# Optimization experiments

Measured on AMD Instinct MI355X. Metric: run time of the kernel, lower is better.

## Reference

```python
import jax, jax.numpy as jnp
import numpy as np

D_MODEL = 1024
D_STATE = 64
HEADDIM = 64
EXPAND = 2
D_INNER = D_MODEL * EXPAND          # 2048
NHEADS = D_INNER // HEADDIM          # 32
D_IN_PROJ = 2 * D_INNER + 2 * D_STATE + NHEADS  # 4256
BATCH, SEQLEN = 4, 4096


def layernorm(x, w, b, eps=1e-5):
    mu = jnp.mean(x, axis=-1, keepdims=True)
    var = jnp.mean(jnp.square(x - mu), axis=-1, keepdims=True)
    return (x - mu) * jax.lax.rsqrt(var + eps) * w + b


def setup_inputs() -> dict:
    key = jax.random.key(0)
    ks = jax.random.split(key, 5)
    x = jax.random.normal(ks[0], (BATCH, SEQLEN, D_MODEL), dtype=jnp.float32)
    # xavier-ish small init (gain 0.5) as in _init_weights
    in_proj_w = jax.random.normal(ks[1], (D_IN_PROJ, D_MODEL), dtype=jnp.float32) * 0.5 * np.sqrt(2.0 / (D_IN_PROJ + D_MODEL))
    out_proj_w = jax.random.normal(ks[2], (D_MODEL, D_INNER), dtype=jnp.float32) * 0.5 * np.sqrt(2.0 / (D_MODEL + D_INNER))
    A_log = jnp.log(jnp.arange(1, NHEADS + 1, dtype=jnp.float32))
    dt_bias = jax.random.normal(ks[3], (NHEADS,), dtype=jnp.float32) * 0.01 + 0.1
    Dparam = jnp.ones((NHEADS,), dtype=jnp.float32)
    return {
        'x': x, 'in_proj_w': in_proj_w, 'out_proj_w': out_proj_w,
        'A_log': A_log, 'dt_bias': dt_bias, 'Dparam': Dparam,
        'ln_w': jnp.ones((D_INNER,), jnp.float32), 'ln_b': jnp.zeros((D_INNER,), jnp.float32),
        'ni_w': jnp.ones((D_MODEL,), jnp.float32), 'ni_b': jnp.zeros((D_MODEL,), jnp.float32),
        'no_w': jnp.ones((D_MODEL,), jnp.float32), 'no_b': jnp.zeros((D_MODEL,), jnp.float32),
    }


def _selective_scan(x_multi, A, Bm, Cm, dt):
    # x_multi: [B,L,H,P], A: [H], Bm/Cm: [B,L,N], dt: [B,L,H]
    Bb, L, H, P = x_multi.shape
    N = Bm.shape[-1]
    dA = jnp.minimum(jnp.exp(dt * A[None, None, :]), 0.99)  # [B,L,H]

    def step(h, inp):
        x_t, B_t, C_t, dA_t = inp  # [B,H,P], [B,N], [B,N], [B,H]
        dBx = jnp.einsum('bhp,bn->bhpn', x_t, B_t)
        h = jnp.clip(dA_t[:, :, None, None] * h + dBx, -10.0, 10.0)
        y_t = jnp.einsum('bn,bhpn->bhp', C_t, h)
        return h, y_t

    h0 = jnp.zeros((Bb, H, P, N), dtype=x_multi.dtype)
    xs = (jnp.moveaxis(x_multi, 1, 0), jnp.moveaxis(Bm, 1, 0),
          jnp.moveaxis(Cm, 1, 0), jnp.moveaxis(dA, 1, 0))
    _, y = jax.lax.scan(step, h0, xs)  # y: [L,B,H,P]
    return jnp.moveaxis(y, 0, 1)


def reference(x, in_proj_w, out_proj_w, A_log, dt_bias, Dparam,
              ln_w, ln_b, ni_w, ni_b, no_w, no_b):
    Bb, L, Dm = x.shape
    x_norm = layernorm(x, ni_w, ni_b)
    zxbcdt = jnp.einsum('bld,ed->ble', x_norm, in_proj_w)  # [B,L,D_IN_PROJ]
    z = zxbcdt[..., :D_INNER]
    x_ssm = zxbcdt[..., D_INNER:2 * D_INNER]
    Bm = zxbcdt[..., 2 * D_INNER:2 * D_INNER + D_STATE]
    Cm = zxbcdt[..., 2 * D_INNER + D_STATE:2 * D_INNER + 2 * D_STATE]
    dt = zxbcdt[..., 2 * D_INNER + 2 * D_STATE:]
    dt = jnp.clip(jax.nn.softplus(dt + dt_bias[None, None, :]), 0.001, 0.1)  # [B,L,H]
    A = -jnp.exp(A_log)  # [H]
    x_multi = x_ssm.reshape(Bb, L, NHEADS, HEADDIM)
    y = _selective_scan(x_multi, A, Bm, Cm, dt)  # [B,L,H,P]
    y = y + x_multi * Dparam[None, None, :, None]  # D skip
    y = y.reshape(Bb, L, D_INNER)
    y = y * jax.nn.silu(z)
    y = layernorm(y, ln_w, ln_b)
    y = jnp.einsum('ble,de->bld', y, out_proj_w)
    y = jnp.clip(y, -10.0, 10.0)
    y = layernorm(y, no_w, no_b)
    return y
```

## Files before the change

kernel.cpp:

```cpp
#include <hip/hip_runtime.h>
#include <hip/hip_bf16.h>
#include <stdint.h>

typedef _Float16 F16;
typedef F16 f16x8 __attribute__((ext_vector_type(8)));
typedef F16 f16x4 __attribute__((ext_vector_type(4)));
typedef float f32x4 __attribute__((ext_vector_type(4)));

#define NTOK   16384
#define DMODEL 1024
#define DINNER 2048
#define DSTATE 64
#define NHEADS 32
#define DINPRJ 4256
#define SEQLEN_ 4096
#define SEGLEN 128
#define NSEG   32

__device__ __forceinline__ void load_lds16(const void* g, void* l) {
  __builtin_amdgcn_global_load_lds((__attribute__((address_space(1))) void*)g,
                                   (__attribute__((address_space(3))) void*)l,
                                   16, 0, 0);
}

__device__ __forceinline__ void lds_st8(F16* base, int row, int col, int rowbytes, f16x8 v) {
  int by = (row * rowbytes + col * 2) ^ ((row & 7) << 4);
  *(f16x8*)((char*)base + by) = v;
}
__device__ __forceinline__ void lds_st1(F16* base, int row, int col, int rowbytes, F16 v) {
  int by = (row * rowbytes + col * 2) ^ ((row & 7) << 4);
  *(F16*)((char*)base + by) = v;
}
__device__ __forceinline__ f16x8 lds_ld8(const F16* base, int row, int col, int rowbytes) {
  int by = (row * rowbytes + col * 2) ^ ((row & 7) << 4);
  return *(const f16x8*)((const char*)base + by);
}

__global__ __launch_bounds__(256) void cvt_kernel(const float* __restrict__ src,
                                                  F16* __restrict__ dst, int n4) {
  int i = blockIdx.x * 256 + threadIdx.x;
  if (i >= n4) return;
  float4 v = *(const float4*)(src + (size_t)i * 4);
  f16x4 o = { (F16)v.x, (F16)v.y, (F16)v.z, (F16)v.w };
  *(f16x4*)(dst + (size_t)i * 4) = o;
}

__device__ __forceinline__ void blk_reduce2(float& s, float& ss) {
  __shared__ float red[8];
#pragma unroll
  for (int m = 32; m >= 1; m >>= 1) { s += __shfl_xor(s, m, 64); ss += __shfl_xor(ss, m, 64); }
  int tid = threadIdx.x, wv = tid >> 6;
  if ((tid & 63) == 0) { red[wv * 2] = s; red[wv * 2 + 1] = ss; }
  __syncthreads();
  s  = red[0] + red[2] + red[4] + red[6];
  ss = red[1] + red[3] + red[5] + red[7];
}

__global__ __launch_bounds__(256) void ln_in_kernel(const float* __restrict__ x,
                                                    const float* __restrict__ w,
                                                    const float* __restrict__ b,
                                                    F16* __restrict__ out) {
  int row = blockIdx.x, tid = threadIdx.x;
  const float* xr = x + (size_t)row * DMODEL + tid * 4;
  float4 v = *(const float4*)xr;
  float s = v.x + v.y + v.z + v.w;
  float ss = v.x * v.x + v.y * v.y + v.z * v.z + v.w * v.w;
  blk_reduce2(s, ss);
  float mu = s * (1.f / DMODEL);
  float var = ss * (1.f / DMODEL) - mu * mu;
  float rs = rsqrtf(var + 1e-5f);
  float4 wv = *(const float4*)(w + tid * 4);
  float4 bv = *(const float4*)(b + tid * 4);
  f16x4 o;
  o.x = (F16)((v.x - mu) * rs * wv.x + bv.x);
  o.y = (F16)((v.y - mu) * rs * wv.y + bv.y);
  o.z = (F16)((v.z - mu) * rs * wv.z + bv.z);
  o.w = (F16)((v.w - mu) * rs * wv.w + bv.w);
  *(f16x4*)(out + (size_t)row * DMODEL + tid * 4) = o;
}

template<int KD, int EPI>
__global__ __launch_bounds__(256)
void gemm_kernel(const F16* __restrict__ A, const F16* __restrict__ W, int Nw,
                 F16* __restrict__ Z, F16* __restrict__ XS,
                 float* __restrict__ BC, float* __restrict__ DT,
                 float* __restrict__ O1)
{
  __shared__ __align__(16) F16 Alds[128 * 64];
  __shared__ __align__(16) F16 Blds[128 * 64];
  const int tid = threadIdx.x;
  const int lane = tid & 63;
  const int wid = tid >> 6;
  const int wm = wid >> 1, wn = wid & 1;
  const int id = blockIdx.x;
  const int bx = (id & 7) * 16 + ((id >> 3) & 15);
  const int by = id >> 7;
  const int m0 = bx * 128, n0 = by * 128;
  const int lr = lane & 15, lk = lane >> 4;

  f32x4 acc[4][4];
#pragma unroll
  for (int i = 0; i < 4; ++i)
#pragma unroll
    for (int j = 0; j < 4; ++j) acc[i][j] = f32x4{0.f, 0.f, 0.f, 0.f};

  for (int k0 = 0; k0 < KD; k0 += 64) {
#pragma unroll
    for (int it = 0; it < 4; ++it) {
      const int q = it * 256 + tid;
      const int row = q >> 3, c = q & 7;
      const int cl = c ^ (row & 7);
      load_lds16(A + (size_t)(m0 + row) * KD + k0 + cl * 8, &Alds[q * 8]);
      int wr = n0 + row; if (wr >= Nw) wr = Nw - 1;
      load_lds16(W + (size_t)wr * KD + k0 + cl * 8, &Blds[q * 8]);
    }
    __syncthreads();
#pragma unroll
    for (int kk = 0; kk < 2; ++kk) {
      const int cs = ((kk * 4 + lk) ^ (lr & 7)) * 8;
      f16x8 af[4], bfr[4];
#pragma unroll
      for (int m = 0; m < 4; ++m)
        af[m] = *(const f16x8*)&Alds[(wm * 64 + m * 16 + lr) * 64 + cs];
#pragma unroll
      for (int n = 0; n < 4; ++n)
        bfr[n] = *(const f16x8*)&Blds[(wn * 64 + n * 16 + lr) * 64 + cs];
#pragma unroll
      for (int m = 0; m < 4; ++m)
#pragma unroll
        for (int n = 0; n < 4; ++n)
          acc[m][n] = __builtin_amdgcn_mfma_f32_16x16x32_f16(af[m], bfr[n], acc[m][n], 0, 0, 0);
    }
    __syncthreads();
  }

#pragma unroll
  for (int m = 0; m < 4; ++m) {
#pragma unroll
    for (int n = 0; n < 4; ++n) {
      int r0 = m0 + wm * 64 + m * 16 + lk * 4;
      int c  = n0 + wn * 64 + n * 16 + lr;
#pragma unroll
      for (int j = 0; j < 4; ++j) {
        float v = acc[m][n][j];
        size_t r = (size_t)(r0 + j);
        if (EPI == 1) {
          O1[r * 1024 + c] = v;
        } else {
          if (c < 2048)        Z[r * 2048 + c] = (F16)v;
          else if (c < 4096)   XS[r * 2048 + (c - 2048)] = (F16)v;
          else if (c < 4160)   BC[r * 128 + (c - 4096)] = v;
          else if (c < 4224)   BC[r * 128 + 64 + (c - 4160)] = v;
          else if (c < 4256)   DT[r * 32 + (c - 4224)] = v;
        }
      }
    }
  }
}

__global__ __launch_bounds__(256) void da_kernel(float* __restrict__ dtraw,
                                                 const float* __restrict__ dt_bias,
                                                 const float* __restrict__ A_log) {
  int idx = blockIdx.x * 256 + threadIdx.x;
  int h = idx & 31;
  float v = dtraw[idx] + dt_bias[h];
  float sp = (v > 20.f) ? v : log1pf(expf(v));
  float dt = fminf(fmaxf(sp, 0.001f), 0.1f);
  float Ah = -expf(A_log[h]);
  dtraw[idx] = fminf(dt * Ah, -0.01005034f);
}

__global__ __launch_bounds__(128) void la_kernel(const float* __restrict__ LD,
                                                 float* __restrict__ LA) {
  const int bh = blockIdx.x, seg = blockIdx.y;
  const int b = bh >> 5, h = bh & 31;
  const int t = threadIdx.x, lane = t & 63;
  size_t tok = (size_t)b * SEQLEN_ + (size_t)seg * SEGLEN + t;
  float v = LD[tok * 32 + h];
#pragma unroll
  for (int m = 1; m <= 32; m <<= 1) {
    float o = __shfl_up(v, m, 64);
    if (lane >= m) v += o;
  }
  __shared__ float w0tot;
  if (t == 63) w0tot = v;
  __syncthreads();
  if (t >= 64) v += w0tot;
  LA[(size_t)bh * SEQLEN_ + (size_t)seg * SEGLEN + t] = v;
}

__global__ __launch_bounds__(256) void ssd_kernel(const float* __restrict__ BC,
                                                  const float* __restrict__ LA,
                                                  F16* __restrict__ XS,
                                                  const float* __restrict__ Dparam,
                                                  F16* __restrict__ HLOC) {
  __shared__ __align__(16) F16 Cb[128 * 64];
  __shared__ __align__(16) F16 Bb[128 * 64];
  __shared__ __align__(16) F16 Xb[64 * 128];
  __shared__ __align__(16) F16 Mm[128 * 128];
  const int h = blockIdx.x, seg = blockIdx.y, b = blockIdx.z;
  const int tid = threadIdx.x, lane = tid & 63, w = tid >> 6;
  const int lr = lane & 15, lk = lane >> 4;
  const int bh = b * 32 + h;
  const size_t tok0 = (size_t)b * SEQLEN_ + (size_t)seg * SEGLEN;
  const float* la = LA + (size_t)bh * SEQLEN_ + (size_t)seg * SEGLEN;

  {
    const int t = tid >> 1, half = tid & 1;
    const float* srcB = BC + (tok0 + t) * 128 + half * 32;
    const float* srcC = srcB + 64;
#pragma unroll
    for (int i = 0; i < 4; ++i) {
      float4 b0 = *(const float4*)(srcB + i * 8);
      float4 b1 = *(const float4*)(srcB + i * 8 + 4);
      float4 c0 = *(const float4*)(srcC + i * 8);
      float4 c1 = *(const float4*)(srcC + i * 8 + 4);
      f16x8 bo = { (F16)b0.x, (F16)b0.y, (F16)b0.z, (F16)b0.w,
                   (F16)b1.x, (F16)b1.y, (F16)b1.z, (F16)b1.w };
      f16x8 co = { (F16)c0.x, (F16)c0.y, (F16)c0.z, (F16)c0.w,
                   (F16)c1.x, (F16)c1.y, (F16)c1.z, (F16)c1.w };
      lds_st8(Bb, t, half * 32 + i * 8, 128, bo);
      lds_st8(Cb, t, half * 32 + i * 8, 128, co);
    }
  }
#pragma unroll
  for (int pass = 0; pass < 4; ++pass) {
    const int srel = tid & 31, oct = tid >> 5;
    const int s = pass * 32 + srel;
    f16x8 xv = *(const f16x8*)(XS + (tok0 + s) * 2048 + h * 64 + oct * 8);
#pragma unroll
    for (int i = 0; i < 8; ++i)
      lds_st1(Xb, oct * 8 + i, s, 256, xv[i]);
  }
  __syncthreads();

  f32x4 g[2][8];
#pragma unroll
  for (int m = 0; m < 2; ++m)
#pragma unroll
    for (int n = 0; n < 8; ++n) g[m][n] = f32x4{0.f, 0.f, 0.f, 0.f};
#pragma unroll
  for (int kk = 0; kk < 2; ++kk) {
    f16x8 a0 = lds_ld8(Cb, w * 32 + lr,      kk * 32 + lk * 8, 128);
    f16x8 a1 = lds_ld8(Cb, w * 32 + 16 + lr, kk * 32 + lk * 8, 128);
#pragma unroll
    for (int n = 0; n < 8; ++n) {
      f16x8 bq = lds_ld8(Bb, n * 16 + lr, kk * 32 + lk * 8, 128);
      g[0][n] = __builtin_amdgcn_mfma_f32_16x16x32_f16(a0, bq, g[0][n], 0, 0, 0);
      g[1][n] = __builtin_amdgcn_mfma_f32_16x16x32_f16(a1, bq, g[1][n], 0, 0, 0);
    }
  }
  const float Dh = Dparam[h];
  float lat[2][4];
#pragma unroll
  for (int m = 0; m < 2; ++m)
#pragma unroll
    for (int j = 0; j < 4; ++j)
      lat[m][j] = la[w * 32 + m * 16 + lk * 4 + j];
#pragma unroll
  for (int n = 0; n < 8; ++n) {
    const int s = n * 16 + lr;
    const float las = la[s];
#pragma unroll
    for (int m = 0; m < 2; ++m)
#pragma unroll
      for (int j = 0; j < 4; ++j) {
        const int t = w * 32 + m * 16 + lk * 4 + j;
        float v = (s <= t) ? g[m][n][j] * __expf(lat[m][j] - las) : 0.f;
        if (s == t) v += Dh;
        lds_st1(Mm, t, s, 256, (F16)v);
      }
  }
  __syncthreads();

  f32x4 y[2][4];
#pragma unroll
  for (int m = 0; m < 2; ++m)
#pragma unroll
    for (int n = 0; n < 4; ++n) y[m][n] = f32x4{0.f, 0.f, 0.f, 0.f};
#pragma unroll
  for (int kk = 0; kk < 4; ++kk) {
    f16x8 a0 = lds_ld8(Mm, w * 32 + lr,      kk * 32 + lk * 8, 256);
    f16x8 a1 = lds_ld8(Mm, w * 32 + 16 + lr, kk * 32 + lk * 8, 256);
#pragma unroll
    for (int n = 0; n < 4; ++n) {
      f16x8 bq = lds_ld8(Xb, n * 16 + lr, kk * 32 + lk * 8, 256);
      y[0][n] = __builtin_amdgcn_mfma_f32_16x16x32_f16(a0, bq, y[0][n], 0, 0, 0);
      y[1][n] = __builtin_amdgcn_mfma_f32_16x16x32_f16(a1, bq, y[1][n], 0, 0, 0);
    }
  }
#pragma unroll
  for (int m = 0; m < 2; ++m)
#pragma unroll
    for (int n = 0; n < 4; ++n)
#pragma unroll
      for (int j = 0; j < 4; ++j) {
        const int t = w * 32 + m * 16 + lk * 4 + j;
        const int p = n * 16 + lr;
        XS[(tok0 + t) * 2048 + h * 64 + p] = (F16)y[m][n][j];
      }
  __syncthreads();

  {
    const int s = tid >> 1, half = tid & 1;
    const float dec = __expf(la[127] - la[s]);
    const float* srcB = BC + (tok0 + s) * 128 + half * 32;
#pragma unroll
    for (int i = 0; i < 4; ++i) {
      float4 b0 = *(const float4*)(srcB + i * 8);
      float4 b1 = *(const float4*)(srcB + i * 8 + 4);
      float vv[8] = { b0.x, b0.y, b0.z, b0.w, b1.x, b1.y, b1.z, b1.w };
#pragma unroll
      for (int q = 0; q < 8; ++q)
        lds_st1(Mm, half * 32 + i * 8 + q, s, 256, (F16)(vv[q] * dec));
    }
  }
  __syncthreads();

  f32x4 hh[4];
#pragma unroll
  for (int n = 0; n < 4; ++n) hh[n] = f32x4{0.f, 0.f, 0.f, 0.f};
#pragma unroll
  for (int kk = 0; kk < 4; ++kk) {
    f16x8 a = lds_ld8(Xb, w * 16 + lr, kk * 32 + lk * 8, 256);
#pragma unroll
    for (int n = 0; n < 4; ++n) {
      f16x8 bq = lds_ld8(Mm, n * 16 + lr, kk * 32 + lk * 8, 256);
      hh[n] = __builtin_amdgcn_mfma_f32_16x16x32_f16(a, bq, hh[n], 0, 0, 0);
    }
  }
  F16* dst = HLOC + ((size_t)bh * NSEG + seg) * 4096;
#pragma unroll
  for (int n = 0; n < 4; ++n)
#pragma unroll
    for (int j = 0; j < 4; ++j) {
      const int p = w * 16 + lk * 4 + j;
      dst[p * 64 + n * 16 + lr] = (F16)hh[n][j];
    }
}

__global__ __launch_bounds__(256) void combine_kernel(F16* __restrict__ HLOC,
                                                      const float* __restrict__ LA) {
  const int bh = blockIdx.x, tid = threadIdx.x;
  const int p = tid >> 2, n0 = (tid & 3) * 16;
  F16* base = HLOC + (size_t)bh * NSEG * 4096 + p * 64 + n0;
  const float* la = LA + (size_t)bh * SEQLEN_;
  union U16 { uint4 v[2]; F16 h[16]; };
  float r[16];
#pragma unroll
  for (int i = 0; i < 16; ++i) r[i] = 0.f;
  for (int k = 0; k < NSEG; ++k) {
    F16* slot = base + (size_t)k * 4096;
    U16 hl; hl.v[0] = *(const uint4*)slot; hl.v[1] = *((const uint4*)slot + 1);
    float P = __expf(la[k * SEGLEN + SEGLEN - 1]);
    U16 ob;
#pragma unroll
    for (int i = 0; i < 16; ++i) ob.h[i] = (F16)r[i];
    *(uint4*)slot = ob.v[0]; *((uint4*)slot + 1) = ob.v[1];
#pragma unroll
    for (int i = 0; i < 16; ++i) r[i] = fmaf(P, r[i], (float)hl.h[i]);
  }
}

__global__ __launch_bounds__(256) void corr_kernel(const float* __restrict__ BC,
                                                   const float* __restrict__ LA,
                                                   const F16* __restrict__ HLOC,
                                                   F16* __restrict__ XS) {
  __shared__ __align__(16) F16 Cd[128 * 72];
  __shared__ __align__(16) F16 Hb[64 * 72];
  const int seg = blockIdx.x, h = blockIdx.y, b = blockIdx.z;
  const int tid = threadIdx.x;
  const size_t tok0 = (size_t)b * SEQLEN_ + (size_t)seg * SEGLEN;
  const int bh = b * 32 + h;
  {
    int t = tid >> 1, half = tid & 1;
    float Dv = __expf(LA[(size_t)bh * SEQLEN_ + seg * SEGLEN + t]);
    const float* src = BC + (tok0 + t) * 128 + 64 + half * 32;
    F16* dstp = &Cd[t * 72 + half * 32];
#pragma unroll
    for (int i = 0; i < 4; ++i) {
      float4 v0 = *(const float4*)(src + i * 8);
      float4 v1 = *(const float4*)(src + i * 8 + 4);
      f16x8 o = { (F16)(Dv * v0.x), (F16)(Dv * v0.y), (F16)(Dv * v0.z), (F16)(Dv * v0.w),
                  (F16)(Dv * v1.x), (F16)(Dv * v1.y), (F16)(Dv * v1.z), (F16)(Dv * v1.w) };
      *(f16x8*)(dstp + i * 8) = o;
    }
  }
  {
    int p = tid >> 2, nn = (tid & 3) * 16;
    const F16* src = HLOC + ((size_t)bh * NSEG + seg) * 4096 + p * 64 + nn;
    uint4 a0 = *(const uint4*)src, a1 = *((const uint4*)src + 1);
    *(uint4*)&Hb[p * 72 + nn] = a0;
    *(uint4*)&Hb[p * 72 + nn + 8] = a1;
  }
  __syncthreads();
  const int lane = tid & 63, w = tid >> 6;
  const int lr = lane & 15, lk = lane >> 4;
  f32x4 acc[2][4];
#pragma unroll
  for (int m = 0; m < 2; ++m)
#pragma unroll
    for (int n = 0; n < 4; ++n) acc[m][n] = f32x4{0.f, 0.f, 0.f, 0.f};
#pragma unroll
  for (int kk = 0; kk < 2; ++kk) {
    f16x8 a0 = *(const f16x8*)&Cd[(w * 32 + lr) * 72 + kk * 32 + lk * 8];
    f16x8 a1 = *(const f16x8*)&Cd[(w * 32 + 16 + lr) * 72 + kk * 32 + lk * 8];
#pragma unroll
    for (int n = 0; n < 4; ++n) {
      f16x8 bq = *(const f16x8*)&Hb[(n * 16 + lr) * 72 + kk * 32 + lk * 8];
      acc[0][n] = __builtin_amdgcn_mfma_f32_16x16x32_f16(a0, bq, acc[0][n], 0, 0, 0);
      acc[1][n] = __builtin_amdgcn_mfma_f32_16x16x32_f16(a1, bq, acc[1][n], 0, 0, 0);
    }
  }
#pragma unroll
  for (int m = 0; m < 2; ++m)
#pragma unroll
    for (int n = 0; n < 4; ++n)
#pragma unroll
      for (int j = 0; j < 4; ++j) {
        int t = w * 32 + m * 16 + lk * 4 + j;
        int p = n * 16 + lr;
        F16* yp = XS + (tok0 + t) * 2048 + h * 64 + p;
        *yp = (F16)((float)*yp + acc[m][n][j]);
      }
}

__global__ __launch_bounds__(256) void silu_ln_kernel(F16* __restrict__ Y,
                                                      const F16* __restrict__ Z,
                                                      const float* __restrict__ lnw,
                                                      const float* __restrict__ lnb) {
  int row = blockIdx.x, tid = threadIdx.x;
  size_t base = (size_t)row * DINNER + tid * 8;
  union { uint4 v; F16 h[8]; } yb, zb, ob;
  yb.v = *(const uint4*)(Y + base);
  zb.v = *(const uint4*)(Z + base);
  float vv[8];
  float s = 0.f, ss = 0.f;
#pragma unroll
  for (int i = 0; i < 8; ++i) {
    float y = (float)yb.h[i];
    float z = (float)zb.h[i];
    float sg = 1.f / (1.f + expf(-z));
    float v = y * z * sg;
    vv[i] = v; s += v; ss += v * v;
  }
  blk_reduce2(s, ss);
  float mu = s * (1.f / DINNER);
  float var = ss * (1.f / DINNER) - mu * mu;
  float rs = rsqrtf(var + 1e-5f);
#pragma unroll
  for (int i = 0; i < 8; ++i) {
    float w = lnw[tid * 8 + i], b = lnb[tid * 8 + i];
    ob.h[i] = (F16)((vv[i] - mu) * rs * w + b);
  }
  *(uint4*)(Y + base) = ob.v;
}

__global__ __launch_bounds__(256) void final_ln_kernel(float* __restrict__ O1,
                                                       const float* __restrict__ w,
                                                       const float* __restrict__ b) {
  int row = blockIdx.x, tid = threadIdx.x;
  size_t base = (size_t)row * DMODEL + tid * 4;
  float4 v = *(const float4*)(O1 + base);
  v.x = fminf(fmaxf(v.x, -10.f), 10.f);
  v.y = fminf(fmaxf(v.y, -10.f), 10.f);
  v.z = fminf(fmaxf(v.z, -10.f), 10.f);
  v.w = fminf(fmaxf(v.w, -10.f), 10.f);
  float s = v.x + v.y + v.z + v.w;
  float ss = v.x * v.x + v.y * v.y + v.z * v.z + v.w * v.w;
  blk_reduce2(s, ss);
  float mu = s * (1.f / DMODEL);
  float var = ss * (1.f / DMODEL) - mu * mu;
  float rs = rsqrtf(var + 1e-5f);
  float4 wv = *(const float4*)(w + tid * 4);
  float4 bv = *(const float4*)(b + tid * 4);
  float4 o;
  o.x = (v.x - mu) * rs * wv.x + bv.x;
  o.y = (v.y - mu) * rs * wv.y + bv.y;
  o.z = (v.z - mu) * rs * wv.z + bv.z;
  o.w = (v.w - mu) * rs * wv.w + bv.w;
  *(float4*)(O1 + base) = o;
}

extern "C" void kernel_launch(void* const* d_in, const int* in_sizes, int n_in,
                              void* d_out, int out_size, void* d_ws, size_t ws_size,
                              hipStream_t stream) {
  const float* x       = (const float*)d_in[0];
  const float* w1      = (const float*)d_in[1];
  const float* w2      = (const float*)d_in[2];
  const float* A_log   = (const float*)d_in[3];
  const float* dt_bias = (const float*)d_in[4];
  const float* Dparam  = (const float*)d_in[5];
  const float* ln_w    = (const float*)d_in[6];
  const float* ln_b    = (const float*)d_in[7];
  const float* ni_w    = (const float*)d_in[8];
  const float* ni_b    = (const float*)d_in[9];
  const float* no_w    = (const float*)d_in[10];
  const float* no_b    = (const float*)d_in[11];

  const size_t NEEDED = 119865344ull;
  if (ws_size < NEEDED) return;

  char* wsb = (char*)d_ws;
  F16*   XS   = (F16*)  (wsb + 0ull);
  float* BC   = (float*)(wsb + 67108864ull);
  float* DT   = (float*)(wsb + 75497472ull);
  F16*   XN   = (F16*)  (wsb + 77594624ull);
  F16*   W2F  = (F16*)  (wsb + 77594624ull);
  F16*   HLOC = (F16*)  (wsb + 81788928ull);
  float* LA   = (float*)(wsb + 115343360ull);
  F16*   W1F  = (F16*)  (wsb + 111149056ull);

  F16*   Z   = (F16*)d_out;
  float* O1  = (float*)d_out;

  cvt_kernel<<<4256, 256, 0, stream>>>(w1, W1F, (DINPRJ * DMODEL) / 4);
  ln_in_kernel<<<NTOK, 256, 0, stream>>>(x, ni_w, ni_b, XN);
  gemm_kernel<1024, 0><<<128 * 34, 256, 0, stream>>>(
      XN, W1F, DINPRJ, Z, XS, BC, DT, nullptr);
  cvt_kernel<<<2048, 256, 0, stream>>>(w2, W2F, (DMODEL * DINNER) / 4);
  da_kernel<<<(NTOK * 32) / 256, 256, 0, stream>>>(DT, dt_bias, A_log);
  la_kernel<<<dim3(128, NSEG), 128, 0, stream>>>(DT, LA);
  ssd_kernel<<<dim3(32, NSEG, 4), 256, 0, stream>>>(BC, LA, XS, Dparam, HLOC);
  combine_kernel<<<128, 256, 0, stream>>>(HLOC, LA);
  corr_kernel<<<dim3(NSEG, 32, 4), 256, 0, stream>>>(BC, LA, HLOC, XS);
  silu_ln_kernel<<<NTOK, 256, 0, stream>>>(XS, Z, ln_w, ln_b);
  gemm_kernel<2048, 1><<<128 * 8, 256, 0, stream>>>(
      XS, W2F, 1024, nullptr, nullptr, nullptr, nullptr, O1);
  final_ln_kernel<<<NTOK, 256, 0, stream>>>(O1, no_w, no_b);
}
```

Measured before the change: 544.2 us.

## Double-buffer GEMM with 256x256 tiles and store B/C projections in fp16

The GEMM moves from 128x128 tiles with 256 threads to 256x256 tiles with 512 threads (8 waves), and a double-buffered LDS pipeline overlaps the next K-slice load with the current MFMA work using explicit vmcnt waits and barriers. B and C projections are now written as fp16 rather than fp32, which halves their traffic and removes the conversion in the ssd and corr kernels. The larger tiles raise data reuse, but they need 128 KB of LDS per block and more accumulator registers. With that much LDS the launch_bounds hint of 2 blocks per CU may not be reachable. The 256-wide N tile also adds wasted work on the ragged 4256 edge.

Result: faster. 513.3 us (-5.7%).

```diff
diff --git a/kernel.cpp b/kernel.cpp
--- a/kernel.cpp
+++ b/kernel.cpp
@@ -80,77 +80,116 @@
 }
 
 template<int KD, int EPI>
-__global__ __launch_bounds__(256)
+__global__ __launch_bounds__(512, 2)
 void gemm_kernel(const F16* __restrict__ A, const F16* __restrict__ W, int Nw,
                  F16* __restrict__ Z, F16* __restrict__ XS,
-                 float* __restrict__ BC, float* __restrict__ DT,
+                 F16* __restrict__ BCH, float* __restrict__ DT,
                  float* __restrict__ O1)
 {
-  __shared__ __align__(16) F16 Alds[128 * 64];
-  __shared__ __align__(16) F16 Blds[128 * 64];
+  constexpr int NT = KD / 64;
+  __shared__ __align__(16) F16 Ab[2][256 * 64];
+  __shared__ __align__(16) F16 Bb[2][256 * 64];
   const int tid = threadIdx.x;
   const int lane = tid & 63;
   const int wid = tid >> 6;
-  const int wm = wid >> 1, wn = wid & 1;
+  const int wm = wid >> 2, wn = wid & 3;
+  const int cpx = gridDim.x >> 3;
   const int id = blockIdx.x;
-  const int bx = (id & 7) * 16 + ((id >> 3) & 15);
-  const int by = id >> 7;
-  const int m0 = bx * 128, n0 = by * 128;
+  const int swz = (id & 7) * cpx + (id >> 3);
+  const int m0 = (swz & 63) * 256, n0 = (swz >> 6) * 256;
   const int lr = lane & 15, lk = lane >> 4;
 
-  f32x4 acc[4][4];
-#pragma unroll
-  for (int i = 0; i < 4; ++i)
+  f32x4 acc[8][4];
+#pragma unroll
+  for (int i = 0; i < 8; ++i)
 #pragma unroll
     for (int j = 0; j < 4; ++j) acc[i][j] = f32x4{0.f, 0.f, 0.f, 0.f};
 
-  for (int k0 = 0; k0 < KD; k0 += 64) {
-#pragma unroll
-    for (int it = 0; it < 4; ++it) {
-      const int q = it * 256 + tid;
-      const int row = q >> 3, c = q & 7;
-      const int cl = c ^ (row & 7);
-      load_lds16(A + (size_t)(m0 + row) * KD + k0 + cl * 8, &Alds[q * 8]);
-      int wr = n0 + row; if (wr >= Nw) wr = Nw - 1;
-      load_lds16(W + (size_t)wr * KD + k0 + cl * 8, &Blds[q * 8]);
-    }
-    __syncthreads();
-#pragma unroll
-    for (int kk = 0; kk < 2; ++kk) {
-      const int cs = ((kk * 4 + lk) ^ (lr & 7)) * 8;
-      f16x8 af[4], bfr[4];
-#pragma unroll
-      for (int m = 0; m < 4; ++m)
-        af[m] = *(const f16x8*)&Alds[(wm * 64 + m * 16 + lr) * 64 + cs];
-#pragma unroll
-      for (int n = 0; n < 4; ++n)
-        bfr[n] = *(const f16x8*)&Blds[(wn * 64 + n * 16 + lr) * 64 + cs];
-#pragma unroll
-      for (int m = 0; m < 4; ++m)
-#pragma unroll
-        for (int n = 0; n < 4; ++n)
-          acc[m][n] = __builtin_amdgcn_mfma_f32_16x16x32_f16(af[m], bfr[n], acc[m][n], 0, 0, 0);
-    }
-    __syncthreads();
-  }
-
-#pragma unroll
-  for (int m = 0; m < 4; ++m) {
-#pragma unroll
-    for (int n = 0; n < 4; ++n) {
-      int r0 = m0 + wm * 64 + m * 16 + lk * 4;
-      int c  = n0 + wn * 64 + n * 16 + lr;
+#define STAGE(T, BUF)                                                          \
+  {                                                                            \
+    const int k0s = (T) * 64;                                                  \
+    _Pragma("unroll")                                                          \
+    for (int i = 0; i < 4; ++i) {                                              \
+      const int u = i * 512 + tid;                                             \
+      const int row = u >> 3;                                                  \
+      const int cl = (u & 7) ^ (row & 7);                                      \
+      load_lds16(A + (size_t)(m0 + row) * KD + k0s + cl * 8, &Ab[BUF][u * 8]); \
+    }                                                                          \
+    _Pragma("unroll")                                                          \
+    for (int i = 0; i < 4; ++i) {                                              \
+      const int u = i * 512 + tid;                                             \
+      const int row = u >> 3;                                                  \
+      const int cl = (u & 7) ^ (row & 7);                                      \
+      int wr = n0 + row; if (wr >= Nw) wr = Nw - 1;                            \
+      load_lds16(W + (size_t)wr * KD + k0s + cl * 8, &Bb[BUF][u * 8]);         \
+    }                                                                          \
+  }
+
+  STAGE(0, 0);
+  for (int t = 0; t < NT; ++t) {
+    const int cur = t & 1;
+    if (t + 1 < NT) {
+      STAGE(t + 1, cur ^ 1);
+      __builtin_amdgcn_sched_barrier(0);
+      asm volatile("s_waitcnt vmcnt(8)" ::: "memory");
+    } else {
+      __builtin_amdgcn_sched_barrier(0);
+      asm volatile("s_waitcnt vmcnt(0)" ::: "memory");
+    }
+    __builtin_amdgcn_sched_barrier(0);
+    __builtin_amdgcn_s_barrier();
+    __builtin_amdgcn_sched_barrier(0);
+
+    const F16* Ac = Ab[cur];
+    const F16* Bc = Bb[cur];
+    f16x8 bfr[4][2];
+#pragma unroll
+    for (int nf = 0; nf < 4; ++nf)
+#pragma unroll
+      for (int kk = 0; kk < 2; ++kk)
+        bfr[nf][kk] = *(const f16x8*)&Bc[(wn * 64 + nf * 16 + lr) * 64 +
+                                         (((kk * 4 + lk) ^ (lr & 7)) * 8)];
+#pragma unroll
+    for (int mf2 = 0; mf2 < 4; ++mf2) {
+      f16x8 af[2][2];
+#pragma unroll
+      for (int q = 0; q < 2; ++q)
+#pragma unroll
+        for (int kk = 0; kk < 2; ++kk)
+          af[q][kk] = *(const f16x8*)&Ac[(wm * 128 + (mf2 * 2 + q) * 16 + lr) * 64 +
+                                         (((kk * 4 + lk) ^ (lr & 7)) * 8)];
+#pragma unroll
+      for (int q = 0; q < 2; ++q)
+#pragma unroll
+        for (int nf = 0; nf < 4; ++nf)
+#pragma unroll
+          for (int kk = 0; kk < 2; ++kk)
+            acc[mf2 * 2 + q][nf] = __builtin_amdgcn_mfma_f32_16x16x32_f16(
+                af[q][kk], bfr[nf][kk], acc[mf2 * 2 + q][nf], 0, 0, 0);
+    }
+    __builtin_amdgcn_sched_barrier(0);
+    __builtin_amdgcn_s_barrier();
+    __builtin_amdgcn_sched_barrier(0);
+  }
+#undef STAGE
+
+#pragma unroll
+  for (int mf = 0; mf < 8; ++mf) {
+#pragma unroll
+    for (int nf = 0; nf < 4; ++nf) {
+      int r0 = m0 + wm * 128 + mf * 16 + lk * 4;
+      int c  = n0 + wn * 64 + nf * 16 + lr;
 #pragma unroll
       for (int j = 0; j < 4; ++j) {
-        float v = acc[m][n][j];
+        float v = acc[mf][nf][j];
         size_t r = (size_t)(r0 + j);
         if (EPI == 1) {
           O1[r * 1024 + c] = v;
         } else {
           if (c < 2048)        Z[r * 2048 + c] = (F16)v;
           else if (c < 4096)   XS[r * 2048 + (c - 2048)] = (F16)v;
-          else if (c < 4160)   BC[r * 128 + (c - 4096)] = v;
-          else if (c < 4224)   BC[r * 128 + 64 + (c - 4160)] = v;
+          else if (c < 4160)   BCH[r * 128 + (c - 4096)] = (F16)v;
+          else if (c < 4224)   BCH[r * 128 + 64 + (c - 4160)] = (F16)v;
           else if (c < 4256)   DT[r * 32 + (c - 4224)] = v;
         }
       }
@@ -189,7 +228,7 @@
   LA[(size_t)bh * SEQLEN_ + (size_t)seg * SEGLEN + t] = v;
 }
 
-__global__ __launch_bounds__(256) void ssd_kernel(const float* __restrict__ BC,
+__global__ __launch_bounds__(256) void ssd_kernel(const F16* __restrict__ BCH,
                                                   const float* __restrict__ LA,
                                                   F16* __restrict__ XS,
                                                   const float* __restrict__ Dparam,
@@ -207,20 +246,12 @@
 
   {
     const int t = tid >> 1, half = tid & 1;
-    const float* srcB = BC + (tok0 + t) * 128 + half * 32;
-    const float* srcC = srcB + 64;
+    const F16* srcB = BCH + (tok0 + t) * 128 + half * 32;
+    const F16* srcC = srcB + 64;
 #pragma unroll
     for (int i = 0; i < 4; ++i) {
-      float4 b0 = *(const float4*)(srcB + i * 8);
-      float4 b1 = *(const float4*)(srcB + i * 8 + 4);
-      float4 c0 = *(const float4*)(srcC + i * 8);
-      float4 c1 = *(const float4*)(srcC + i * 8 + 4);
-      f16x8 bo = { (F16)b0.x, (F16)b0.y, (F16)b0.z, (F16)b0.w,
-                   (F16)b1.x, (F16)b1.y, (F16)b1.z, (F16)b1.w };
-      f16x8 co = { (F16)c0.x, (F16)c0.y, (F16)c0.z, (F16)c0.w,
-                   (F16)c1.x, (F16)c1.y, (F16)c1.z, (F16)c1.w };
-      lds_st8(Bb, t, half * 32 + i * 8, 128, bo);
-      lds_st8(Cb, t, half * 32 + i * 8, 128, co);
+      lds_st8(Bb, t, half * 32 + i * 8, 128, *(const f16x8*)(srcB + i * 8));
+      lds_st8(Cb, t, half * 32 + i * 8, 128, *(const f16x8*)(srcC + i * 8));
     }
   }
 #pragma unroll
@@ -304,15 +335,13 @@
   {
     const int s = tid >> 1, half = tid & 1;
     const float dec = __expf(la[127] - la[s]);
-    const float* srcB = BC + (tok0 + s) * 128 + half * 32;
+    const F16* srcB = BCH + (tok0 + s) * 128 + half * 32;
 #pragma unroll
     for (int i = 0; i < 4; ++i) {
-      float4 b0 = *(const float4*)(srcB + i * 8);
-      float4 b1 = *(const float4*)(srcB + i * 8 + 4);
-      float vv[8] = { b0.x, b0.y, b0.z, b0.w, b1.x, b1.y, b1.z, b1.w };
+      f16x8 bv = *(const f16x8*)(srcB + i * 8);
 #pragma unroll
       for (int q = 0; q < 8; ++q)
-        lds_st1(Mm, half * 32 + i * 8 + q, s, 256, (F16)(vv[q] * dec));
+        lds_st1(Mm, half * 32 + i * 8 + q, s, 256, (F16)((float)bv[q] * dec));
     }
   }
   __syncthreads();
@@ -362,7 +391,7 @@
   }
 }
 
-__global__ __launch_bounds__(256) void corr_kernel(const float* __restrict__ BC,
+__global__ __launch_bounds__(256) void corr_kernel(const F16* __restrict__ BCH,
                                                    const float* __restrict__ LA,
                                                    const F16* __restrict__ HLOC,
                                                    F16* __restrict__ XS) {
@@ -375,14 +404,14 @@
   {
     int t = tid >> 1, half = tid & 1;
     float Dv = __expf(LA[(size_t)bh * SEQLEN_ + seg * SEGLEN + t]);
-    const float* src = BC + (tok0 + t) * 128 + 64 + half * 32;
+    const F16* src = BCH + (tok0 + t) * 128 + 64 + half * 32;
     F16* dstp = &Cd[t * 72 + half * 32];
 #pragma unroll
     for (int i = 0; i < 4; ++i) {
-      float4 v0 = *(const float4*)(src + i * 8);
-      float4 v1 = *(const float4*)(src + i * 8 + 4);
-      f16x8 o = { (F16)(Dv * v0.x), (F16)(Dv * v0.y), (F16)(Dv * v0.z), (F16)(Dv * v0.w),
-                  (F16)(Dv * v1.x), (F16)(Dv * v1.y), (F16)(Dv * v1.z), (F16)(Dv * v1.w) };
+      f16x8 cv = *(const f16x8*)(src + i * 8);
+      f16x8 o;
+#pragma unroll
+      for (int q = 0; q < 8; ++q) o[q] = (F16)(Dv * (float)cv[q]);
       *(f16x8*)(dstp + i * 8) = o;
     }
   }
@@ -503,7 +532,7 @@
 
   char* wsb = (char*)d_ws;
   F16*   XS   = (F16*)  (wsb + 0ull);
-  float* BC   = (float*)(wsb + 67108864ull);
+  F16*   BCH  = (F16*)  (wsb + 67108864ull);
   float* DT   = (float*)(wsb + 75497472ull);
   F16*   XN   = (F16*)  (wsb + 77594624ull);
   F16*   W2F  = (F16*)  (wsb + 77594624ull);
@@ -516,16 +545,16 @@
 
   cvt_kernel<<<4256, 256, 0, stream>>>(w1, W1F, (DINPRJ * DMODEL) / 4);
   ln_in_kernel<<<NTOK, 256, 0, stream>>>(x, ni_w, ni_b, XN);
-  gemm_kernel<1024, 0><<<128 * 34, 256, 0, stream>>>(
-      XN, W1F, DINPRJ, Z, XS, BC, DT, nullptr);
+  gemm_kernel<1024, 0><<<64 * 17, 512, 0, stream>>>(
+      XN, W1F, DINPRJ, Z, XS, BCH, DT, nullptr);
   cvt_kernel<<<2048, 256, 0, stream>>>(w2, W2F, (DMODEL * DINNER) / 4);
   da_kernel<<<(NTOK * 32) / 256, 256, 0, stream>>>(DT, dt_bias, A_log);
   la_kernel<<<dim3(128, NSEG), 128, 0, stream>>>(DT, LA);
-  ssd_kernel<<<dim3(32, NSEG, 4), 256, 0, stream>>>(BC, LA, XS, Dparam, HLOC);
+  ssd_kernel<<<dim3(32, NSEG, 4), 256, 0, stream>>>(BCH, LA, XS, Dparam, HLOC);
   combine_kernel<<<128, 256, 0, stream>>>(HLOC, LA);
-  corr_kernel<<<dim3(NSEG, 32, 4), 256, 0, stream>>>(BC, LA, HLOC, XS);
+  corr_kernel<<<dim3(NSEG, 32, 4), 256, 0, stream>>>(BCH, LA, HLOC, XS);
   silu_ln_kernel<<<NTOK, 256, 0, stream>>>(XS, Z, ln_w, ln_b);
-  gemm_kernel<2048, 1><<<128 * 8, 256, 0, stream>>>(
+  gemm_kernel<2048, 1><<<64 * 4, 512, 0, stream>>>(
       XS, W2F, 1024, nullptr, nullptr, nullptr, nullptr, O1);
   final_ln_kernel<<<NTOK, 256, 0, stream>>>(O1, no_w, no_b);
 }
```
